# Optimization experiments

Hardware: AMD Instinct MI355X
Metric: run time of the kernel (lower is better)

Reference implementation:

```python
import jax, jax.numpy as jnp
import numpy as np

SQ, B, NP, HN = 2048, 2, 16, 64  # [seq, batch, heads, head_dim]

def setup_inputs() -> dict:
    key = jax.random.key(0)
    kq, kk, kv = jax.random.split(key, 3)
    return {
        "query": jax.random.normal(kq, (SQ, B, NP, HN), dtype=jnp.float32),
        "key":   jax.random.normal(kk, (SQ, B, NP, HN), dtype=jnp.float32),
        "value": jax.random.normal(kv, (SQ, B, NP, HN), dtype=jnp.float32),
    }

def reference(query, key, value):
    sq, b, nheads, hn = query.shape
    # NOTE: original module computes norm_factor=sqrt(hn) but never applies it;
    # scores are UNscaled QK^T, replicated faithfully here.
    scores = jnp.einsum('sbnh,tbnh->bnst', query, key)          # [b, np, sq, sk]
    probs = jax.nn.softmax(scores, axis=-1)                      # mask=None -> plain softmax
    # dropout is deterministic (train=False default) -> identity
    context = jnp.einsum('bnst,tbnh->sbnh', probs, value)        # [sq, b, np, hn]
    return context.reshape(sq, b, nheads * hn).astype(jnp.float32)
```

## Files before the change

kernel.cpp:

```cpp
#include <hip/hip_runtime.h>
#include <math.h>
#include <stdint.h>

#define SQ 2048
#define NBH 32
#define HN 64
#define BQ 128
#define BK 64
#define BK2 128
#define NP2 (SQ/BK2)
#define TOK 2048
#define HSTRIDE (SQ*HN)

typedef _Float16 half2v __attribute__((ext_vector_type(2)));
typedef _Float16 half4v __attribute__((ext_vector_type(4)));
typedef _Float16 half8v __attribute__((ext_vector_type(8)));
typedef float f32x16 __attribute__((ext_vector_type(16)));

__device__ __forceinline__ void async16(const void* g, void* l) {
  __builtin_amdgcn_global_load_lds(
      (const __attribute__((address_space(1))) void*)g,
      (__attribute__((address_space(3))) void*)l, 16, 0, 0);
}

__device__ __forceinline__ float fexp2(float x) {
#if __has_builtin(__builtin_amdgcn_exp2f)
  return __builtin_amdgcn_exp2f(x);
#else
  return exp2f(x);
#endif
}

__global__ __launch_bounds__(256) void prep_kv(const float* __restrict__ K,
                                               const float* __restrict__ V,
                                               _Float16* __restrict__ Kh,
                                               _Float16* __restrict__ Vt) {
  __shared__ _Float16 vs[HN * 64];
  const int t = threadIdx.x;
  const int head = blockIdx.y;
  {
    const int key = blockIdx.x * 64 + (t >> 2);
    const int c0 = (t & 3) * 2;
    const float* src = K + (size_t)key * TOK + head * HN + c0 * 8;
    float4 a = *(const float4*)src;
    float4 b = *(const float4*)(src + 4);
    float4 c = *(const float4*)(src + 8);
    float4 d = *(const float4*)(src + 12);
    half8v h0, h1;
    h0[0]=(_Float16)a.x; h0[1]=(_Float16)a.y; h0[2]=(_Float16)a.z; h0[3]=(_Float16)a.w;
    h0[4]=(_Float16)b.x; h0[5]=(_Float16)b.y; h0[6]=(_Float16)b.z; h0[7]=(_Float16)b.w;
    h1[0]=(_Float16)c.x; h1[1]=(_Float16)c.y; h1[2]=(_Float16)c.z; h1[3]=(_Float16)c.w;
    h1[4]=(_Float16)d.x; h1[5]=(_Float16)d.y; h1[6]=(_Float16)d.z; h1[7]=(_Float16)d.w;
    _Float16* row = Kh + (size_t)head * HSTRIDE + (size_t)key * 64;
    *(half8v*)&row[((c0    ) ^ (key & 7)) * 8] = h0;
    *(half8v*)&row[((c0 + 1) ^ (key & 7)) * 8] = h1;
  }
  {
    const int kt = blockIdx.x * 64;
    const int kl = (t >> 3) * 2;
    const int db = (t & 7) * 8;
    const float* src = V + (size_t)(kt + kl) * TOK + head * HN + db;
    float4 a0 = *(const float4*)src;
    float4 a1 = *(const float4*)(src + 4);
    float4 b0 = *(const float4*)(src + TOK);
    float4 b1 = *(const float4*)(src + TOK + 4);
    const float av[8] = {a0.x,a0.y,a0.z,a0.w,a1.x,a1.y,a1.z,a1.w};
    const float bv[8] = {b0.x,b0.y,b0.z,b0.w,b1.x,b1.y,b1.z,b1.w};
    const int u = kl >> 2;
    #pragma unroll
    for (int j = 0; j < 8; ++j) {
      const int dim = db + j;
      const int pos = u ^ (dim & 15);
      half2v h; h[0] = (_Float16)av[j]; h[1] = (_Float16)bv[j];
      *(half2v*)&vs[dim * 64 + pos * 4 + (kl & 3)] = h;
    }
    __syncthreads();
    const int dim = t >> 2;
    const int q = (t & 3) ^ (dim & 3);
    const _Float16* srow = &vs[dim * 64 + q * 16];
    _Float16* drow = Vt + (size_t)head * HSTRIDE + (size_t)dim * SQ + kt + q * 16;
    *(half8v*)&drow[0] = *(const half8v*)&srow[0];
    *(half8v*)&drow[8] = *(const half8v*)&srow[8];
  }
}

__global__ __launch_bounds__(256, 2)
void fattn_mfma(const float* __restrict__ Q, const _Float16* __restrict__ Kh,
                const _Float16* __restrict__ Vt, float* __restrict__ O) {
  __shared__ __align__(16) _Float16 kbf[2][2 * BK * 64];
  __shared__ __align__(16) _Float16 vtf[2][2 * HN * 64];

  const int t = threadIdx.x;
  const int lane = t & 63;
  const int w = t >> 6;
  const int h2 = lane >> 5;
  const int l31 = lane & 31;
  const int q0 = blockIdx.x * BQ + w * 32;
  const int head = blockIdx.y;
  const _Float16* Kp = Kh + (size_t)head * HSTRIDE;
  const _Float16* Vp = Vt + (size_t)head * HSTRIDE;

  half8v qf[4];
  {
    const float* qp = Q + (size_t)(q0 + l31) * TOK + head * HN + 8 * h2;
    const float s = 1.44269504088896f;
    #pragma unroll
    for (int ks = 0; ks < 4; ++ks) {
      float4 a = *(const float4*)(qp + 16 * ks);
      float4 b = *(const float4*)(qp + 16 * ks + 4);
      half8v f;
      f[0] = (_Float16)(s*a.x); f[1] = (_Float16)(s*a.y); f[2] = (_Float16)(s*a.z); f[3] = (_Float16)(s*a.w);
      f[4] = (_Float16)(s*b.x); f[5] = (_Float16)(s*b.y); f[6] = (_Float16)(s*b.z); f[7] = (_Float16)(s*b.w);
      qf[ks] = f;
    }
  }

  f32x16 acc0, acc1;
  #pragma unroll
  for (int r = 0; r < 16; ++r) { acc0[r] = 0.f; acc1[r] = 0.f; }
  float m_i = -INFINITY, l_i = 0.f;

  auto stage = [&](int p) {
    const int buf = p & 1;
    const size_t kt = (size_t)p * BK2;
    #pragma unroll
    for (int i = 0; i < 4; ++i) {
      const int off = w * 512 + i * 2048;
      async16(Kp + kt * 64 + off + lane * 8, &kbf[buf][off]);
    }
    #pragma unroll
    for (int tl = 0; tl < 2; ++tl)
      #pragma unroll
      for (int i = 0; i < 2; ++i) {
        const int off = w * 1024 + i * 512;
        const int eo = off + lane * 8;
        const int dim = eo >> 6, inner = eo & 63;
        async16(Vp + (size_t)dim * SQ + kt + tl * 64 + inner,
                &vtf[buf][tl * 4096 + off]);
      }
  };

  stage(0);
  for (int p = 0; p < NP2; ++p) {
    __syncthreads();
    if (p + 1 < NP2) stage(p + 1);
    const int cur = p & 1;

    f32x16 sa0, sa1, sb0, sb1;
    {
      f32x16 c0, c1, d0, d1;
      #pragma unroll
      for (int r = 0; r < 16; ++r) { c0[r]=0.f; c1[r]=0.f; d0[r]=0.f; d1[r]=0.f; }
      #pragma unroll
      for (int ks = 0; ks < 4; ++ks) {
        const int pos = ((h2 + 2 * ks) ^ (l31 & 7)) * 8;
        half8v a0v = *(const half8v*)&kbf[cur][l31 * 64 + pos];
        half8v a1v = *(const half8v*)&kbf[cur][(l31 + 32) * 64 + pos];
        half8v b0v = *(const half8v*)&kbf[cur][4096 + l31 * 64 + pos];
        half8v b1v = *(const half8v*)&kbf[cur][4096 + (l31 + 32) * 64 + pos];
        c0 = __builtin_amdgcn_mfma_f32_32x32x16_f16(a0v, qf[ks], c0, 0, 0, 0);
        c1 = __builtin_amdgcn_mfma_f32_32x32x16_f16(a1v, qf[ks], c1, 0, 0, 0);
        d0 = __builtin_amdgcn_mfma_f32_32x32x16_f16(b0v, qf[ks], d0, 0, 0, 0);
        d1 = __builtin_amdgcn_mfma_f32_32x32x16_f16(b1v, qf[ks], d1, 0, 0, 0);
      }
      sa0 = c0; sa1 = c1; sb0 = d0; sb1 = d1;
    }

    float mx = -INFINITY;
    #pragma unroll
    for (int r = 0; r < 16; ++r)
      mx = fmaxf(mx, fmaxf(fmaxf(sa0[r], sa1[r]), fmaxf(sb0[r], sb1[r])));
    mx = fmaxf(mx, __shfl_xor(mx, 32, 64));
    const float mnew = fmaxf(m_i, mx);
    const float alpha = fexp2(m_i - mnew);
    float rsum = 0.f;
    #pragma unroll
    for (int r = 0; r < 16; ++r) {
      float p0 = fexp2(sa0[r] - mnew);
      float p1 = fexp2(sa1[r] - mnew);
      float p2 = fexp2(sb0[r] - mnew);
      float p3 = fexp2(sb1[r] - mnew);
      sa0[r] = p0; sa1[r] = p1; sb0[r] = p2; sb1[r] = p3;
      rsum += (p0 + p1) + (p2 + p3);
    }
    rsum += __shfl_xor(rsum, 32, 64);
    l_i = l_i * alpha + rsum;
    m_i = mnew;
    #pragma unroll
    for (int r = 0; r < 16; ++r) { acc0[r] *= alpha; acc1[r] *= alpha; }

    #pragma unroll
    for (int tl = 0; tl < 2; ++tl) {
      const int vbase = tl * 4096;
      #pragma unroll
      for (int ks = 0; ks < 4; ++ks) {
        const int rb = 8 * (ks & 1);
        const f32x16& s = tl ? ((ks < 2) ? sb0 : sb1) : ((ks < 2) ? sa0 : sa1);
        union { half8v v8; half2v v2[4]; } pu;
        #pragma unroll
        for (int tt = 0; tt < 4; ++tt) {
          auto pk = __builtin_amdgcn_cvt_pkrtz(s[rb + 2 * tt], s[rb + 2 * tt + 1]);
          pu.v2[tt] = *(half2v*)&pk;
        }
        #pragma unroll
        for (int mbd = 0; mbd < 2; ++mbd) {
          const int dim = l31 + 32 * mbd;
          const int sw = dim & 15;
          union { half8v v8; half4v v4[2]; } au;
          au.v4[0] = *(const half4v*)&vtf[cur][vbase + dim * 64 + ((4 * ks + h2)     ^ sw) * 4];
          au.v4[1] = *(const half4v*)&vtf[cur][vbase + dim * 64 + ((4 * ks + 2 + h2) ^ sw) * 4];
          if (mbd == 0)
            acc0 = __builtin_amdgcn_mfma_f32_32x32x16_f16(au.v8, pu.v8, acc0, 0, 0, 0);
          else
            acc1 = __builtin_amdgcn_mfma_f32_32x32x16_f16(au.v8, pu.v8, acc1, 0, 0, 0);
        }
      }
    }
  }

  const float invl = 1.f / l_i;
  float* orow = O + (size_t)(q0 + l31) * TOK + head * HN;
  #pragma unroll
  for (int r = 0; r < 16; ++r) {
    const int d = (r & 3) + 8 * (r >> 2) + 4 * h2;
    orow[d]      = acc0[r] * invl;
    orow[d + 32] = acc1[r] * invl;
  }
}

extern "C" void kernel_launch(void* const* d_in, const int* in_sizes, int n_in,
                              void* d_out, int out_size, void* d_ws, size_t ws_size,
                              hipStream_t stream) {
  const float* Q = (const float*)d_in[0];
  const float* K = (const float*)d_in[1];
  const float* V = (const float*)d_in[2];
  float* O = (float*)d_out;
  _Float16* Kh = (_Float16*)d_ws;
  _Float16* Vh = Kh + (size_t)NBH * HSTRIDE;
  prep_kv<<<dim3(SQ / 64, NBH), 256, 0, stream>>>(K, V, Kh, Vh);
  fattn_mfma<<<dim3(SQ / BQ, NBH), 256, 0, stream>>>(Q, Kh, Vh, O);
}
```

Baseline: 142.7 us.

## Split key tiles across two wave groups per block and merge softmax partials

Doubles the block to 512 threads, with two wave groups that each take half of every 128-key tile (64 keys each) for the same 128 queries. At the end the two partial accumulators are merged through shared memory with a log-sum-exp rescale. This halves per-wave score registers and raises the number of waves per CU, aiming for better latency hiding. It also swaps the cross-half shuffle reductions for permlane32_swap where that builtin exists, at the cost of an extra LDS merge and barrier at the end.

After: 143.0 us. Within noise of the previous version (+0.2%).

```diff
diff --git a/kernel.cpp b/kernel.cpp
--- a/kernel.cpp
+++ b/kernel.cpp
@@ -6,7 +6,6 @@
 #define NBH 32
 #define HN 64
 #define BQ 128
-#define BK 64
 #define BK2 128
 #define NP2 (SQ/BK2)
 #define TOK 2048
@@ -28,6 +27,25 @@
   return __builtin_amdgcn_exp2f(x);
 #else
   return exp2f(x);
+#endif
+}
+
+__device__ __forceinline__ float xmax32(float x) {
+#if __has_builtin(__builtin_amdgcn_permlane32_swap)
+  auto r = __builtin_amdgcn_permlane32_swap(__float_as_int(x), __float_as_int(x),
+                                            false, false);
+  return fmaxf(__int_as_float(r[0]), __int_as_float(r[1]));
+#else
+  return fmaxf(x, __shfl_xor(x, 32, 64));
+#endif
+}
+__device__ __forceinline__ float xadd32(float x) {
+#if __has_builtin(__builtin_amdgcn_permlane32_swap)
+  auto r = __builtin_amdgcn_permlane32_swap(__float_as_int(x), __float_as_int(x),
+                                            false, false);
+  return __int_as_float(r[0]) + __int_as_float(r[1]);
+#else
+  return x + __shfl_xor(x, 32, 64);
 #endif
 }
 
@@ -84,21 +102,25 @@
   }
 }
 
-__global__ __launch_bounds__(256, 2)
+__global__ __launch_bounds__(512, 4)
 void fattn_mfma(const float* __restrict__ Q, const _Float16* __restrict__ Kh,
                 const _Float16* __restrict__ Vt, float* __restrict__ O) {
-  __shared__ __align__(16) _Float16 kbf[2][2 * BK * 64];
-  __shared__ __align__(16) _Float16 vtf[2][2 * HN * 64];
+  __shared__ __align__(16) _Float16 smem[4 * 8192];
+  _Float16* kbf = smem;
+  _Float16* vtf = smem + 16384;
 
   const int t = threadIdx.x;
   const int lane = t & 63;
   const int w = t >> 6;
+  const int qw = w & 3;
+  const int g = w >> 2;
   const int h2 = lane >> 5;
   const int l31 = lane & 31;
-  const int q0 = blockIdx.x * BQ + w * 32;
+  const int q0 = blockIdx.x * BQ + qw * 32;
   const int head = blockIdx.y;
   const _Float16* Kp = Kh + (size_t)head * HSTRIDE;
   const _Float16* Vp = Vt + (size_t)head * HSTRIDE;
+  const int tb = g * 4096;
 
   half8v qf[4];
   {
@@ -124,20 +146,18 @@
     const int buf = p & 1;
     const size_t kt = (size_t)p * BK2;
     #pragma unroll
-    for (int i = 0; i < 4; ++i) {
-      const int off = w * 512 + i * 2048;
-      async16(Kp + kt * 64 + off + lane * 8, &kbf[buf][off]);
-    }
-    #pragma unroll
-    for (int tl = 0; tl < 2; ++tl)
-      #pragma unroll
-      for (int i = 0; i < 2; ++i) {
-        const int off = w * 1024 + i * 512;
-        const int eo = off + lane * 8;
-        const int dim = eo >> 6, inner = eo & 63;
-        async16(Vp + (size_t)dim * SQ + kt + tl * 64 + inner,
-                &vtf[buf][tl * 4096 + off]);
-      }
+    for (int i = 0; i < 2; ++i) {
+      const int off = w * 512 + i * 4096;
+      async16(Kp + kt * 64 + off + lane * 8, kbf + buf * 8192 + off);
+    }
+    #pragma unroll
+    for (int tl = 0; tl < 2; ++tl) {
+      const int off = w * 512;
+      const int eo = off + lane * 8;
+      const int dim = eo >> 6, inner = eo & 63;
+      async16(Vp + (size_t)dim * SQ + kt + tl * 64 + inner,
+              vtf + buf * 8192 + tl * 4096 + off);
+    }
   };
 
   stage(0);
@@ -145,86 +165,102 @@
     __syncthreads();
     if (p + 1 < NP2) stage(p + 1);
     const int cur = p & 1;
-
-    f32x16 sa0, sa1, sb0, sb1;
-    {
-      f32x16 c0, c1, d0, d1;
-      #pragma unroll
-      for (int r = 0; r < 16; ++r) { c0[r]=0.f; c1[r]=0.f; d0[r]=0.f; d1[r]=0.f; }
-      #pragma unroll
-      for (int ks = 0; ks < 4; ++ks) {
-        const int pos = ((h2 + 2 * ks) ^ (l31 & 7)) * 8;
-        half8v a0v = *(const half8v*)&kbf[cur][l31 * 64 + pos];
-        half8v a1v = *(const half8v*)&kbf[cur][(l31 + 32) * 64 + pos];
-        half8v b0v = *(const half8v*)&kbf[cur][4096 + l31 * 64 + pos];
-        half8v b1v = *(const half8v*)&kbf[cur][4096 + (l31 + 32) * 64 + pos];
-        c0 = __builtin_amdgcn_mfma_f32_32x32x16_f16(a0v, qf[ks], c0, 0, 0, 0);
-        c1 = __builtin_amdgcn_mfma_f32_32x32x16_f16(a1v, qf[ks], c1, 0, 0, 0);
-        d0 = __builtin_amdgcn_mfma_f32_32x32x16_f16(b0v, qf[ks], d0, 0, 0, 0);
-        d1 = __builtin_amdgcn_mfma_f32_32x32x16_f16(b1v, qf[ks], d1, 0, 0, 0);
-      }
-      sa0 = c0; sa1 = c1; sb0 = d0; sb1 = d1;
-    }
-
-    float mx = -INFINITY;
-    #pragma unroll
-    for (int r = 0; r < 16; ++r)
-      mx = fmaxf(mx, fmaxf(fmaxf(sa0[r], sa1[r]), fmaxf(sb0[r], sb1[r])));
-    mx = fmaxf(mx, __shfl_xor(mx, 32, 64));
+    const _Float16* kb = kbf + cur * 8192 + tb;
+    const _Float16* vb = vtf + cur * 8192 + tb;
+
+    f32x16 c0, c1;
+    #pragma unroll
+    for (int r = 0; r < 16; ++r) { c0[r] = 0.f; c1[r] = 0.f; }
+    #pragma unroll
+    for (int ks = 0; ks < 4; ++ks) {
+      const int pos = ((h2 + 2 * ks) ^ (l31 & 7)) * 8;
+      half8v a0v = *(const half8v*)&kb[l31 * 64 + pos];
+      half8v a1v = *(const half8v*)&kb[(l31 + 32) * 64 + pos];
+      c0 = __builtin_amdgcn_mfma_f32_32x32x16_f16(a0v, qf[ks], c0, 0, 0, 0);
+      c1 = __builtin_amdgcn_mfma_f32_32x32x16_f16(a1v, qf[ks], c1, 0, 0, 0);
+    }
+
+    float mx0 = fmaxf(c0[0], c1[0]);
+    float mx1 = fmaxf(c0[1], c1[1]);
+    float mx2 = fmaxf(c0[2], c1[2]);
+    float mx3 = fmaxf(c0[3], c1[3]);
+    #pragma unroll
+    for (int r = 4; r < 16; r += 4) {
+      mx0 = fmaxf(mx0, fmaxf(c0[r],     c1[r]));
+      mx1 = fmaxf(mx1, fmaxf(c0[r + 1], c1[r + 1]));
+      mx2 = fmaxf(mx2, fmaxf(c0[r + 2], c1[r + 2]));
+      mx3 = fmaxf(mx3, fmaxf(c0[r + 3], c1[r + 3]));
+    }
+    float mx = fmaxf(fmaxf(mx0, mx1), fmaxf(mx2, mx3));
+    mx = xmax32(mx);
     const float mnew = fmaxf(m_i, mx);
     const float alpha = fexp2(m_i - mnew);
-    float rsum = 0.f;
+    float rs0 = 0.f, rs1 = 0.f;
     #pragma unroll
     for (int r = 0; r < 16; ++r) {
-      float p0 = fexp2(sa0[r] - mnew);
-      float p1 = fexp2(sa1[r] - mnew);
-      float p2 = fexp2(sb0[r] - mnew);
-      float p3 = fexp2(sb1[r] - mnew);
-      sa0[r] = p0; sa1[r] = p1; sb0[r] = p2; sb1[r] = p3;
-      rsum += (p0 + p1) + (p2 + p3);
-    }
-    rsum += __shfl_xor(rsum, 32, 64);
+      float p0 = fexp2(c0[r] - mnew);
+      float p1 = fexp2(c1[r] - mnew);
+      c0[r] = p0; c1[r] = p1;
+      rs0 += p0; rs1 += p1;
+    }
+    float rsum = xadd32(rs0 + rs1);
     l_i = l_i * alpha + rsum;
     m_i = mnew;
     #pragma unroll
     for (int r = 0; r < 16; ++r) { acc0[r] *= alpha; acc1[r] *= alpha; }
 
     #pragma unroll
-    for (int tl = 0; tl < 2; ++tl) {
-      const int vbase = tl * 4096;
+    for (int ks = 0; ks < 4; ++ks) {
+      const int rb = 8 * (ks & 1);
+      const f32x16& s = (ks < 2) ? c0 : c1;
+      union { half8v v8; half2v v2[4]; } pu;
       #pragma unroll
-      for (int ks = 0; ks < 4; ++ks) {
-        const int rb = 8 * (ks & 1);
-        const f32x16& s = tl ? ((ks < 2) ? sb0 : sb1) : ((ks < 2) ? sa0 : sa1);
-        union { half8v v8; half2v v2[4]; } pu;
-        #pragma unroll
-        for (int tt = 0; tt < 4; ++tt) {
-          auto pk = __builtin_amdgcn_cvt_pkrtz(s[rb + 2 * tt], s[rb + 2 * tt + 1]);
-          pu.v2[tt] = *(half2v*)&pk;
-        }
-        #pragma unroll
-        for (int mbd = 0; mbd < 2; ++mbd) {
-          const int dim = l31 + 32 * mbd;
-          const int sw = dim & 15;
-          union { half8v v8; half4v v4[2]; } au;
-          au.v4[0] = *(const half4v*)&vtf[cur][vbase + dim * 64 + ((4 * ks + h2)     ^ sw) * 4];
-          au.v4[1] = *(const half4v*)&vtf[cur][vbase + dim * 64 + ((4 * ks + 2 + h2) ^ sw) * 4];
-          if (mbd == 0)
-            acc0 = __builtin_amdgcn_mfma_f32_32x32x16_f16(au.v8, pu.v8, acc0, 0, 0, 0);
-          else
-            acc1 = __builtin_amdgcn_mfma_f32_32x32x16_f16(au.v8, pu.v8, acc1, 0, 0, 0);
-        }
+      for (int tt = 0; tt < 4; ++tt) {
+        auto pk = __builtin_amdgcn_cvt_pkrtz(s[rb + 2 * tt], s[rb + 2 * tt + 1]);
+        pu.v2[tt] = *(half2v*)&pk;
       }
-    }
-  }
-
-  const float invl = 1.f / l_i;
-  float* orow = O + (size_t)(q0 + l31) * TOK + head * HN;
-  #pragma unroll
-  for (int r = 0; r < 16; ++r) {
-    const int d = (r & 3) + 8 * (r >> 2) + 4 * h2;
-    orow[d]      = acc0[r] * invl;
-    orow[d + 32] = acc1[r] * invl;
+      #pragma unroll
+      for (int mbd = 0; mbd < 2; ++mbd) {
+        const int dim = l31 + 32 * mbd;
+        const int sw = dim & 15;
+        union { half8v v8; half4v v4[2]; } au;
+        au.v4[0] = *(const half4v*)&vb[dim * 64 + ((4 * ks + h2)     ^ sw) * 4];
+        au.v4[1] = *(const half4v*)&vb[dim * 64 + ((4 * ks + 2 + h2) ^ sw) * 4];
+        if (mbd == 0)
+          acc0 = __builtin_amdgcn_mfma_f32_32x32x16_f16(au.v8, pu.v8, acc0, 0, 0, 0);
+        else
+          acc1 = __builtin_amdgcn_mfma_f32_32x32x16_f16(au.v8, pu.v8, acc1, 0, 0, 0);
+      }
+    }
+  }
+
+  __syncthreads();
+  float* fb = (float*)smem;
+  const int slot = qw * 64 + lane;
+  if (g == 1) {
+    #pragma unroll
+    for (int r = 0; r < 16; ++r) {
+      fb[slot * 32 + r]      = acc0[r];
+      fb[slot * 32 + 16 + r] = acc1[r];
+    }
+    fb[8192 + slot] = m_i;
+    fb[8448 + slot] = l_i;
+  }
+  __syncthreads();
+  if (g == 0) {
+    const float m2 = fb[8192 + slot];
+    const float l2 = fb[8448 + slot];
+    const float ms = fmaxf(m_i, m2);
+    const float a0 = fexp2(m_i - ms);
+    const float a1 = fexp2(m2 - ms);
+    const float invl = 1.f / (l_i * a0 + l2 * a1);
+    float* orow = O + (size_t)(q0 + l31) * TOK + head * HN;
+    #pragma unroll
+    for (int r = 0; r < 16; ++r) {
+      const int d = (r & 3) + 8 * (r >> 2) + 4 * h2;
+      orow[d]      = (acc0[r] * a0 + fb[slot * 32 + r]      * a1) * invl;
+      orow[d + 32] = (acc1[r] * a0 + fb[slot * 32 + 16 + r] * a1) * invl;
+    }
   }
 }
 
@@ -238,5 +274,5 @@
   _Float16* Kh = (_Float16*)d_ws;
   _Float16* Vh = Kh + (size_t)NBH * HSTRIDE;
   prep_kv<<<dim3(SQ / 64, NBH), 256, 0, stream>>>(K, V, Kh, Vh);
-  fattn_mfma<<<dim3(SQ / BQ, NBH), 256, 0, stream>>>(Q, Kh, Vh, O);
-}
+  fattn_mfma<<<dim3(SQ / BQ, NBH), 512, 0, stream>>>(Q, Kh, Vh, O);
+}
```
